# Kernel optimization log

Measured on AMD Instinct MI355X. Metric: run time of the kernel, lower is better.

Reference implementation:

```python
import jax, jax.numpy as jnp
import numpy as np
import math

G_GRAPHS = 32   # graphs per batch
NPG = 2048      # nodes per graph
DEG = 8         # avg degree
IN_DIM = 128
HID = 128

def _lin(k, fi, fo):
    return jax.random.normal(k, (fi, fo), jnp.float32) / np.sqrt(fi).astype(np.float32)

def setup_inputs():
    key = jax.random.key(0)
    ks = jax.random.split(key, 32)
    Nt = G_GRAPHS * NPG
    Epg = NPG * DEG
    E = G_GRAPHS * Epg
    x = jax.random.normal(ks[0], (Nt, IN_DIM), jnp.float32)
    src = jax.random.randint(ks[1], (E,), 0, NPG)
    dst = jax.random.randint(ks[2], (E,), 0, NPG)
    off = (jnp.arange(E) // Epg) * NPG  # keep edges within their graph block
    edge_index = jnp.stack([src + off, dst + off]).astype(jnp.int32)
    batch = (jnp.arange(Nt) // NPG).astype(jnp.int32)
    p = {}
    dims = [(IN_DIM, HID), (HID, HID), (HID, HID), (HID, HID)]
    for i, (fi, fo) in enumerate(dims, 1):
        p['Wl%d' % i] = _lin(ks[3 * i], fi, fo)
        p['bl%d' % i] = jnp.zeros((fo,), jnp.float32)
        p['Wr%d' % i] = _lin(ks[3 * i + 1], fi, fo)
    for j in (1, 2):  # SAGPooling score GNN (GraphConv hidden->1)
        p['Prel%d' % j] = _lin(ks[15 + 2 * j], HID, 1)
        p['prb%d' % j] = jnp.zeros((1,), jnp.float32)
        p['Proot%d' % j] = _lin(ks[16 + 2 * j], HID, 1)
    p['W5'] = _lin(ks[24], HID, 64); p['b5'] = jnp.zeros((64,), jnp.float32)
    p['W6'] = _lin(ks[25], 64, 2);  p['b6'] = jnp.zeros((2,), jnp.float32)
    return dict(x=x, edge_index=edge_index, batch=batch, npg=NPG, **p)

def reference(x, edge_index, batch, npg,
              Wl1, bl1, Wr1, Wl2, bl2, Wr2, Wl3, bl3, Wr3, Wl4, bl4, Wr4,
              Prel1, prb1, Proot1, Prel2, prb2, Proot2, W5, b5, W6, b6):
    src, dst = edge_index[0], edge_index[1]
    Nt = x.shape[0]
    Gn = Nt // npg

    def sage(h, em, Wl, bl, Wr):
        # SAGEConv (mean aggr): lin_l(mean_j x_j) + lin_r(x_root)
        s = jax.ops.segment_sum(h[src] * em[:, None], dst, num_segments=Nt)
        c = jax.ops.segment_sum(em, dst, num_segments=Nt)
        return (s / jnp.maximum(c, 1.0)[:, None]) @ Wl + bl + h @ Wr

    def pool(h, em, nm, k, Prel, prb, Proot):
        # SAGPooling: score = GraphConv(h) (add aggr), top-k per graph, x *= tanh(score)
        s = jax.ops.segment_sum(h[src] * em[:, None], dst, num_segments=Nt)
        score = (s @ Prel + h @ Proot + prb)[:, 0]
        smr = jnp.where(nm > 0, score, -1e30).reshape(Gn, npg)
        _, idx = jax.lax.top_k(smr, k)
        newm = jnp.zeros((Gn, npg), h.dtype).at[jnp.arange(Gn)[:, None], idx].set(1.0).reshape(-1)
        h = h * jnp.tanh(score)[:, None] * newm[:, None]
        em = em * newm[src] * newm[dst]  # filter_adj: keep edges with both ends kept
        return h, em, newm

    em = jnp.ones(src.shape, x.dtype)
    nm = jnp.ones((Nt,), x.dtype)
    h = jax.nn.relu(sage(x, em, Wl1, bl1, Wr1))
    h = jax.nn.relu(sage(h, em, Wl2, bl2, Wr2))
    k1 = math.ceil(0.5 * npg)
    h, em, nm = pool(h, em, nm, k1, Prel1, prb1, Proot1)
    h = jax.nn.relu(sage(h, em, Wl3, bl3, Wr3)) * nm[:, None]
    h = jax.nn.relu(sage(h, em, Wl4, bl4, Wr4)) * nm[:, None]
    k2 = math.ceil(0.5 * k1)
    h, em, nm = pool(h, em, nm, k2, Prel2, prb2, Proot2)
    # global mean pool over surviving nodes
    sums = jax.ops.segment_sum(h, batch, num_segments=Gn)
    cnt = jax.ops.segment_sum(nm, batch, num_segments=Gn)
    g = sums / jnp.maximum(cnt, 1.0)[:, None]
    g = jax.nn.relu(g @ W5 + b5)
    return jax.nn.log_softmax(g @ W6 + b6, axis=1)
```

## Files before the change

kernel.cpp:

```cpp
#include <hip/hip_runtime.h>
#include <hip/hip_bf16.h>
#include <math.h>

#define NT   65536
#define NPGC 2048
#define NG   32
#define NE   524288
#define HID  128

typedef short short8 __attribute__((ext_vector_type(8)));
typedef float f32x4  __attribute__((ext_vector_type(4)));

__device__ __forceinline__ float bf2f(unsigned short u) {
    union { unsigned int i; float f; } v; v.i = ((unsigned int)u) << 16; return v.f;
}
__device__ __forceinline__ unsigned short f2bf(float f) {
    union { float f; unsigned int i; } v; v.f = f;
    unsigned int x = v.i;
    return (unsigned short)((x + 0x7fffu + ((x >> 16) & 1u)) >> 16);
}
__device__ __forceinline__ void split2(float v, unsigned short& hi, unsigned short& lo) {
    unsigned int b = __float_as_uint(v);
    hi = (unsigned short)(b >> 16);
    float rem = v - __uint_as_float(b & 0xFFFF0000u);
    lo = (unsigned short)(__float_as_uint(rem) >> 16);
}

__global__ void k_detect(const unsigned short* __restrict__ x, int* __restrict__ flag) {
    __shared__ int cnt;
    if (threadIdx.x == 0) cnt = 0;
    __syncthreads();
    int sane = 0;
#pragma unroll
    for (int j = 0; j < 16; ++j) {
        unsigned short u = x[threadIdx.x * 16 + j];
        int e = (u >> 7) & 0xFF;
        if (e > 0x60 && e < 0xA0) sane++;
    }
    atomicAdd(&cnt, sane);
    __syncthreads();
    if (threadIdx.x == 0) *flag = (cnt > 3686) ? 1 : 0;
}

struct CvtDesc { const void* src[22]; int n[22]; int off[22]; };

__global__ void k_cvt(CvtDesc d, float* __restrict__ wts, const int* __restrict__ flag) {
    int t = blockIdx.y;
    int n = d.n[t];
    bool isbf = (*flag != 0);
    const unsigned short* sb = (const unsigned short*)d.src[t];
    const float* sf = (const float*)d.src[t];
    float* o = wts + d.off[t];
    for (int i = blockIdx.x * blockDim.x + threadIdx.x; i < n; i += gridDim.x * blockDim.x)
        o[i] = isbf ? bf2f(sb[i]) : sf[i];
}

__global__ void k_packW(const float* __restrict__ wts, int4 oWl, int4 oWr,
                        unsigned short* __restrict__ Wpack,
                        int* __restrict__ rowc, int* __restrict__ fill) {
    int idx = blockIdx.x * 256 + threadIdx.x;
    if (idx < NT) { rowc[idx] = 0; fill[idx] = 0; }
    if (idx >= 4 * 8 * 8 * 64 * 8) return;
    int L    = idx >> 15;
    int rem  = idx & 32767;
    int ct   = rem >> 12;
    int rem2 = rem & 4095;
    int ks   = rem2 >> 9;
    int rem3 = rem2 & 511;
    int lane = rem3 >> 3;
    int j    = rem3 & 7;
    int k   = ks * 32 + (lane >> 4) * 8 + j;
    int col = ct * 16 + (lane & 15);
    int ol = (L == 0) ? oWl.x : (L == 1) ? oWl.y : (L == 2) ? oWl.z : oWl.w;
    int orr = (L == 0) ? oWr.x : (L == 1) ? oWr.y : (L == 2) ? oWr.z : oWr.w;
    float w = (k < 128) ? wts[ol + k * 128 + col] : wts[orr + (k - 128) * 128 + col];
    unsigned short hi = f2bf(w);
    unsigned short lo = f2bf(w - bf2f(hi));
    int base = L * 65536 + (ct * 8 + ks) * 512 + lane * 8 + j;
    Wpack[base]         = hi;
    Wpack[base + 32768] = lo;
}

__global__ void k_load_x(const void* __restrict__ x, float* __restrict__ out,
                         const int* __restrict__ flag, int n4,
                         float* __restrict__ nm, const int* __restrict__ dstE,
                         int* __restrict__ rowc) {
    int i = blockIdx.x * blockDim.x + threadIdx.x;
    if (i < NT) nm[i] = 1.0f;
    if (i < NE) atomicAdd(&rowc[dstE[i]], 1);
    if (i >= n4) return;
    if (*flag) {
        ushort4 v = ((const ushort4*)x)[i];
        float4 o;
        o.x = bf2f(v.x); o.y = bf2f(v.y); o.z = bf2f(v.z); o.w = bf2f(v.w);
        ((float4*)out)[i] = o;
    }
}

__global__ void k_scan1(const int* __restrict__ cnt, int* __restrict__ rp, int* __restrict__ bsum,
                        float* __restrict__ invc) {
    __shared__ int s[256];
    int t = threadIdx.x;
    int i = blockIdx.x * 256 + t;
    int v = cnt[i];
    invc[i] = 1.0f / fmaxf((float)v, 1.0f);
    s[t] = v;
    __syncthreads();
    for (int off = 1; off < 256; off <<= 1) {
        int a = (t >= off) ? s[t - off] : 0;
        __syncthreads();
        s[t] += a;
        __syncthreads();
    }
    rp[i] = s[t] - v;
    if (t == 255) bsum[blockIdx.x] = s[255];
}

__global__ void k_scan23(int* __restrict__ rp, const int* __restrict__ bsum) {
    __shared__ int s[256];
    int t = threadIdx.x;
    s[t] = bsum[t];
    __syncthreads();
    for (int off = 1; off < 256; off <<= 1) {
        int a = (t >= off) ? s[t - off] : 0;
        __syncthreads();
        s[t] += a;
        __syncthreads();
    }
    int boffv = s[blockIdx.x] - bsum[blockIdx.x];
    int i = blockIdx.x * 256 + t;
    rp[i] += boffv;
    if (i == 0) rp[NT] = NE;
}

__global__ void k_scatter(const int* __restrict__ src, const int* __restrict__ dst,
                          const int* __restrict__ rp, int* __restrict__ fill, int* __restrict__ col) {
    int e = blockIdx.x * blockDim.x + threadIdx.x;
    if (e < NE) {
        int d = dst[e];
        int p = rp[d] + atomicAdd(&fill[d], 1);
        col[p] = src[e];
    }
}

__global__ void k_invc(const float* __restrict__ nm, const int* __restrict__ rp,
                       const int* __restrict__ col, float* __restrict__ invc) {
    int n = blockIdx.x * 256 + threadIdx.x;
    int beg = rp[n], end = rp[n + 1];
    float c = 0.f;
    for (int e = beg; e < end; ++e) c += nm[col[e]];
    invc[n] = 1.0f / fmaxf(c, 1.0f);
}

__device__ __forceinline__ int lds_sw(int node, int k) {
    int g = k >> 3;
    int go = g ^ (node & 7);
    return node * 128 + go * 8 + (k & 7);
}

template<bool HAS_TS>
__device__ __forceinline__ void sage_body(
    const float* __restrict__ h, const float* __restrict__ ts,
    const float* __restrict__ nm, const float* __restrict__ invc,
    const int* __restrict__ rp, const int* __restrict__ col,
    const unsigned short* __restrict__ Wp,
    unsigned short* Ahi, unsigned short* Alo,
    int n0, int tid, f32x4 acc[2][2])
{
    int lane = tid & 63, w = tid >> 6;
    int lrow = lane & 15, quad = lane >> 4;

#pragma unroll
    for (int pass = 0; pass < 4; ++pass) {
        int node = pass * 8 + (tid >> 5);
        int f = (tid & 31) * 4;
        int gn = n0 + node;
        float ax = 0.f, ay = 0.f, az = 0.f, aw = 0.f;
        if (nm[gn] > 0.f) {
            int beg = rp[gn], end = rp[gn + 1];
            for (int e0 = beg; e0 < end; e0 += 4) {
                int ecl = end - 1;
                int e1 = (e0 + 1 < end) ? e0 + 1 : ecl;
                int e2 = (e0 + 2 < end) ? e0 + 2 : ecl;
                int e3 = (e0 + 3 < end) ? e0 + 3 : ecl;
                int s0 = col[e0], s1 = col[e1], s2 = col[e2], s3 = col[e3];
                float4 v0 = *(const float4*)&h[(size_t)s0 * HID + f];
                float4 v1 = *(const float4*)&h[(size_t)s1 * HID + f];
                float4 v2 = *(const float4*)&h[(size_t)s2 * HID + f];
                float4 v3 = *(const float4*)&h[(size_t)s3 * HID + f];
                float c0 = HAS_TS ? ts[s0] : 1.0f;
                float c1 = (e0 + 1 < end) ? (HAS_TS ? ts[s1] : 1.0f) : 0.0f;
                float c2 = (e0 + 2 < end) ? (HAS_TS ? ts[s2] : 1.0f) : 0.0f;
                float c3 = (e0 + 3 < end) ? (HAS_TS ? ts[s3] : 1.0f) : 0.0f;
                ax += v0.x * c0 + v1.x * c1 + v2.x * c2 + v3.x * c3;
                ay += v0.y * c0 + v1.y * c1 + v2.y * c2 + v3.y * c3;
                az += v0.z * c0 + v1.z * c1 + v2.z * c2 + v3.z * c3;
                aw += v0.w * c0 + v1.w * c1 + v2.w * c2 + v3.w * c3;
            }
        }
        float inv = invc[gn];
        ushort4 hi4, lo4;
        split2(ax * inv, hi4.x, lo4.x);
        split2(ay * inv, hi4.y, lo4.y);
        split2(az * inv, hi4.z, lo4.z);
        split2(aw * inv, hi4.w, lo4.w);
        int a = lds_sw(node, f);
        *(ushort4*)&Ahi[a] = hi4;
        *(ushort4*)&Alo[a] = lo4;
    }
    __syncthreads();

#pragma unroll
    for (int ks = 0; ks < 4; ++ks) {
        short8 bh[2], blo[2];
#pragma unroll
        for (int c = 0; c < 2; ++c) {
            int ct = 2 * w + c;
            bh[c]  = *(const short8*)&Wp[(ct * 8 + ks) * 512 + lane * 8];
            blo[c] = *(const short8*)&Wp[32768 + (ct * 8 + ks) * 512 + lane * 8];
        }
        int kb = ks * 32 + quad * 8;
#pragma unroll
        for (int st = 0; st < 2; ++st) {
            int a = lds_sw(st * 16 + lrow, kb);
            short8 ah = *(const short8*)&Ahi[a];
            short8 al = *(const short8*)&Alo[a];
#pragma unroll
            for (int c = 0; c < 2; ++c) {
                acc[st][c] = __builtin_amdgcn_mfma_f32_16x16x32_bf16(ah, bh[c],  acc[st][c], 0, 0, 0);
                acc[st][c] = __builtin_amdgcn_mfma_f32_16x16x32_bf16(al, bh[c],  acc[st][c], 0, 0, 0);
                acc[st][c] = __builtin_amdgcn_mfma_f32_16x16x32_bf16(ah, blo[c], acc[st][c], 0, 0, 0);
            }
        }
    }
    __syncthreads();

#pragma unroll
    for (int i = 0; i < 4; ++i) {
        int idx = i * 256 + tid;
        int node = idx >> 5;
        int f = (idx & 31) * 4;
        int gn = n0 + node;
        float4 v = *(const float4*)&h[(size_t)gn * HID + f];
        float sc = HAS_TS ? ts[gn] : 1.0f;
        ushort4 hi4, lo4;
        split2(v.x * sc, hi4.x, lo4.x);
        split2(v.y * sc, hi4.y, lo4.y);
        split2(v.z * sc, hi4.z, lo4.z);
        split2(v.w * sc, hi4.w, lo4.w);
        int a = lds_sw(node, f);
        *(ushort4*)&Ahi[a] = hi4;
        *(ushort4*)&Alo[a] = lo4;
    }
    __syncthreads();

#pragma unroll
    for (int ks = 4; ks < 8; ++ks) {
        short8 bh[2], blo[2];
#pragma unroll
        for (int c = 0; c < 2; ++c) {
            int ct = 2 * w + c;
            bh[c]  = *(const short8*)&Wp[(ct * 8 + ks) * 512 + lane * 8];
            blo[c] = *(const short8*)&Wp[32768 + (ct * 8 + ks) * 512 + lane * 8];
        }
        int kb = (ks - 4) * 32 + quad * 8;
#pragma unroll
        for (int st = 0; st < 2; ++st) {
            int a = lds_sw(st * 16 + lrow, kb);
            short8 ah = *(const short8*)&Ahi[a];
            short8 al = *(const short8*)&Alo[a];
#pragma unroll
            for (int c = 0; c < 2; ++c) {
                acc[st][c] = __builtin_amdgcn_mfma_f32_16x16x32_bf16(ah, bh[c],  acc[st][c], 0, 0, 0);
                acc[st][c] = __builtin_amdgcn_mfma_f32_16x16x32_bf16(al, bh[c],  acc[st][c], 0, 0, 0);
                acc[st][c] = __builtin_amdgcn_mfma_f32_16x16x32_bf16(ah, blo[c], acc[st][c], 0, 0, 0);
            }
        }
    }
}

template<bool HAS_TS>
__global__ void __launch_bounds__(256, 8) k_sage_plain(
    const float* __restrict__ h, const void* __restrict__ xraw, const int* __restrict__ flag,
    const float* __restrict__ ts,
    const float* __restrict__ nm, const float* __restrict__ invc,
    const int* __restrict__ rp, const int* __restrict__ col,
    const unsigned short* __restrict__ Wp, const float* __restrict__ bl,
    float* __restrict__ out)
{
    __shared__ unsigned short Ahi[32 * 128];
    __shared__ unsigned short Alo[32 * 128];
    int tid = threadIdx.x;
    int b = blockIdx.x;
    int graph = (b & 7) * 4 + (b >> 9);
    int tile  = (b >> 3) & 63;
    int n0 = graph * NPGC + tile * 32;
    int lane = tid & 63, w = tid >> 6;
    int lrow = lane & 15, quad = lane >> 4;
    f32x4 acc[2][2] = {};

    const float* hh = h;
    if (xraw && *flag == 0) hh = (const float*)xraw;

    sage_body<HAS_TS>(hh, ts, nm, invc, rp, col, Wp, Ahi, Alo, n0, tid, acc);

#pragma unroll
    for (int c = 0; c < 2; ++c) {
        int colg = (2 * w + c) * 16 + lrow;
        float bias = bl[colg];
#pragma unroll
        for (int st = 0; st < 2; ++st) {
#pragma unroll
            for (int rr = 0; rr < 4; ++rr) {
                int node = n0 + st * 16 + quad * 4 + rr;
                float val = fmaxf(acc[st][c][rr] + bias, 0.f) * nm[node];
                out[(size_t)node * HID + colg] = val;
            }
        }
    }
}

__global__ void __launch_bounds__(256, 8) k_sage_dots(
    const float* __restrict__ h,
    const float* __restrict__ nm, const float* __restrict__ invc,
    const int* __restrict__ rp, const int* __restrict__ col,
    const unsigned short* __restrict__ Wp, const float* __restrict__ bl,
    float* __restrict__ out,
    const float* __restrict__ Prel, const float* __restrict__ Proot,
    float* __restrict__ q, float* __restrict__ r)
{
    __shared__ unsigned short Ahi[32 * 128];
    __shared__ unsigned short Alo[32 * 128];
    int tid = threadIdx.x;
    int b = blockIdx.x;
    int graph = (b & 7) * 4 + (b >> 9);
    int tile  = (b >> 3) & 63;
    int n0 = graph * NPGC + tile * 32;
    int lane = tid & 63, w = tid >> 6;
    int lrow = lane & 15, quad = lane >> 4;
    f32x4 acc[2][2] = {};

    sage_body<false>(h, nullptr, nm, invc, rp, col, Wp, Ahi, Alo, n0, tid, acc);

    float qp[2][4] = {}, rp_[2][4] = {};
#pragma unroll
    for (int c = 0; c < 2; ++c) {
        int colg = (2 * w + c) * 16 + lrow;
        float bias = bl[colg];
        float pq = Prel[colg], pr = Proot[colg];
#pragma unroll
        for (int st = 0; st < 2; ++st) {
#pragma unroll
            for (int rr = 0; rr < 4; ++rr) {
                int node = n0 + st * 16 + quad * 4 + rr;
                float val = fmaxf(acc[st][c][rr] + bias, 0.f) * nm[node];
                out[(size_t)node * HID + colg] = val;
                qp[st][rr] += val * pq;
                rp_[st][rr] += val * pr;
            }
        }
    }
#pragma unroll
    for (int st = 0; st < 2; ++st)
#pragma unroll
        for (int rr = 0; rr < 4; ++rr) {
#pragma unroll
            for (int m = 1; m < 16; m <<= 1) {
                qp[st][rr]  += __shfl_xor(qp[st][rr],  m, 64);
                rp_[st][rr] += __shfl_xor(rp_[st][rr], m, 64);
            }
        }
    __syncthreads();
    float* qa = (float*)Ahi;
    if (tid < 64) qa[tid] = 0.f;
    __syncthreads();
    if (lrow == 0) {
#pragma unroll
        for (int st = 0; st < 2; ++st)
#pragma unroll
            for (int rr = 0; rr < 4; ++rr) {
                int nl = st * 16 + quad * 4 + rr;
                atomicAdd(&qa[nl], qp[st][rr]);
                atomicAdd(&qa[32 + nl], rp_[st][rr]);
            }
    }
    __syncthreads();
    if (tid < 32) {
        q[n0 + tid] = qa[tid];
        r[n0 + tid] = qa[32 + tid];
    }
}

__global__ void k_score(const float* __restrict__ q, const float* __restrict__ r,
                        const float* __restrict__ prb,
                        const int* __restrict__ rp, const int* __restrict__ col,
                        float* __restrict__ score) {
    int n = blockIdx.x * 256 + threadIdx.x;
    int beg = rp[n], end = rp[n + 1];
    float s = 0.f;
    for (int e = beg; e < end; ++e) s += q[col[e]];
    score[n] = s + r[n] + prb[0];
}

__global__ void __launch_bounds__(256) k_topk(const float* __restrict__ score,
                                              float* __restrict__ nm,
                                              float* __restrict__ tval, int k) {
    __shared__ unsigned int u[NPGC];
    __shared__ int hist[256];
    __shared__ int scanb[257];
    __shared__ int wtot[4];
    __shared__ unsigned int s_byte;
    __shared__ int s_kk;
    int tid = threadIdx.x;
    int lane = tid & 63, wv = tid >> 6;
    int base = blockIdx.x * NPGC;

    for (int j = tid; j < NPGC; j += 256) {
        float sc = (nm[base + j] > 0.f) ? score[base + j] : -1e30f;
        unsigned int v = __float_as_uint(sc);
        v = (v & 0x80000000u) ? ~v : (v | 0x80000000u);
        u[j] = v;
    }
    hist[tid] = 0;
    if (tid == 0) scanb[256] = 0;
    __syncthreads();

    unsigned int prefix = 0;
    int kk = k;
#pragma unroll
    for (int round = 0; round < 4; ++round) {
        int shift = 24 - 8 * round;
        unsigned int pmask = (round == 0) ? 0u : (0xFFFFFFFFu << (32 - 8 * round));
        for (int j = tid; j < NPGC; j += 256) {
            unsigned int v = u[j];
            if ((v & pmask) == prefix) atomicAdd(&hist[(v >> shift) & 0xFF], 1);
        }
        __syncthreads();
        int s = hist[tid];
#pragma unroll
        for (int off = 1; off < 64; off <<= 1) {
            int t = __shfl_down(s, off, 64);
            s += (lane + off < 64) ? t : 0;
        }
        if (lane == 0) wtot[wv] = s;
        __syncthreads();
        int add = 0;
#pragma unroll
        for (int w2 = 1; w2 < 4; ++w2) add += (wv + w2 < 4) ? wtot[wv + w2] : 0;
        s += add;
        scanb[tid] = s;
        __syncthreads();
        int above = scanb[tid + 1];
        if (s >= kk && above < kk) { s_byte = (unsigned int)tid; s_kk = kk - above; }
        hist[tid] = 0;
        __syncthreads();
        prefix |= (s_byte << shift);
        kk = s_kk;
    }
    unsigned int thr = prefix;

    int j0 = tid * 8;
    int cnt = 0;
#pragma unroll
    for (int j = 0; j < 8; ++j) cnt += (u[j0 + j] == thr);
    int s = cnt;
#pragma unroll
    for (int off = 1; off < 64; off <<= 1) {
        int t = __shfl_up(s, off, 64);
        s += (lane >= off) ? t : 0;
    }
    if (lane == 63) wtot[wv] = s;
    __syncthreads();
    int add = 0;
#pragma unroll
    for (int w2 = 0; w2 < 4; ++w2) add += (w2 < wv) ? wtot[w2] : 0;
    int rank = s - cnt + add;
#pragma unroll
    for (int j = 0; j < 8; ++j) {
        unsigned int v = u[j0 + j];
        bool keep;
        if (v > thr) keep = true;
        else if (v == thr) { keep = (rank < kk); rank++; }
        else keep = false;
        nm[base + j0 + j]   = keep ? 1.0f : 0.0f;
        tval[base + j0 + j] = keep ? tanhf(score[base + j0 + j]) : 0.0f;
    }
}

__global__ void k_gsum(const float* __restrict__ h, const float* __restrict__ t,
                       const float* __restrict__ nm,
                       float* __restrict__ g, float* __restrict__ gcnt) {
    int b = blockIdx.x;
    int graph = b >> 4, part = b & 15;
    int f = threadIdx.x & 127, sub = threadIdx.x >> 7;
    int nbase = graph * NPGC + part * 128 + sub * 64;
    float acc = 0.f;
#pragma unroll 4
    for (int n = 0; n < 64; ++n)
        acc += h[(size_t)(nbase + n) * HID + f] * t[nbase + n];
    atomicAdd(&g[graph * HID + f], acc);
    if (threadIdx.x < 64 && sub == 0) {
        float cnt = 0.f;
        int cb = graph * NPGC + part * 128;
        for (int n = threadIdx.x; n < 128; n += 64) cnt += nm[cb + n];
        for (int o = 32; o > 0; o >>= 1) cnt += __shfl_down(cnt, o, 64);
        if (threadIdx.x == 0) atomicAdd(&gcnt[graph], cnt);
    }
}

__global__ void k_mlp(const float* __restrict__ g, const float* __restrict__ gcnt,
                      const float* __restrict__ W5,
                      const float* __restrict__ b5, const float* __restrict__ W6,
                      const float* __restrict__ b6, void* __restrict__ out,
                      const int* __restrict__ flag) {
    __shared__ float g5[64];
    __shared__ float ls[2];
    int graph = blockIdx.x, j = threadIdx.x;
    float ic = 1.0f / fmaxf(gcnt[graph], 1.0f);
    float acc = b5[j];
    for (int f = 0; f < HID; ++f)
        acc += (g[graph * HID + f] * ic) * W5[f * 64 + j];
    g5[j] = fmaxf(acc, 0.f);
    __syncthreads();
    if (j < 2) {
        float l = b6[j];
        for (int t = 0; t < 64; ++t) l += g5[t] * W6[t * 2 + j];
        ls[j] = l;
    }
    __syncthreads();
    if (j == 0) {
        float a = ls[0], b = ls[1];
        float mx = fmaxf(a, b);
        float lse = mx + logf(expf(a - mx) + expf(b - mx));
        if (*flag) {
            ((unsigned short*)out)[graph * 2 + 0] = f2bf(a - lse);
            ((unsigned short*)out)[graph * 2 + 1] = f2bf(b - lse);
        } else {
            ((float*)out)[graph * 2 + 0] = a - lse;
            ((float*)out)[graph * 2 + 1] = b - lse;
        }
    }
}

extern "C" void kernel_launch(void* const* d_in, const int* in_sizes, int n_in,
                              void* d_out, int out_size, void* d_ws, size_t ws_size,
                              hipStream_t stream) {
    const void* x    = d_in[0];
    const int*  ei   = (const int*)d_in[1];
    const int*  srcE = ei;
    const int*  dstE = ei + NE;

    char* ws = (char*)d_ws;
    float* hA    = (float*)(ws + 0);
    float* hB    = (float*)(ws + 33554432);
    float* tvec  = (float*)(ws + 67108864);
    float* invc  = (float*)(ws + 67371008);
    float* q     = (float*)(ws + 100663296);
    float* r     = (float*)(ws + 100925440);
    float* score = (float*)(ws + 101187584);
    float* nm    = (float*)(ws + 101449728);
    int*   rowc  = (int*)  (ws + 101711872);
    int*   rp    = (int*)  (ws + 101974016);
    int*   bsum  = (int*)  (ws + 102236416);
    int*   fill  = (int*)  (ws + 102238464);
    int*   col   = (int*)  (ws + 102500608);
    float* g     = (float*)(ws + 104597760);
    float* gcnt  = (float*)(ws + 104614144);
    int*   flag  = (int*)  (ws + 104615936);
    float* wts   = (float*)(ws + 104616960);
    unsigned short* Wpack = (unsigned short*)(ws + 105179136);
    (void)in_sizes; (void)n_in; (void)out_size; (void)ws_size;

    const int O_Wl1 = 0,      O_bl1 = 16384,  O_Wr1 = 16512;
    const int O_Wl2 = 32896,  O_bl2 = 49280,  O_Wr2 = 49408;
    const int O_Wl3 = 65792,  O_bl3 = 82176,  O_Wr3 = 82304;
    const int O_Wl4 = 98688,  O_bl4 = 115072, O_Wr4 = 115200;
    const int O_Pr1 = 131584, O_pb1 = 131712, O_Po1 = 131713;
    const int O_Pr2 = 131841, O_pb2 = 131969, O_Po2 = 131970;
    const int O_W5  = 132098, O_b5  = 140290, O_W6 = 140354, O_b6 = 140482;

    CvtDesc d;
    const int srcIdx[22] = {4,5,6,7,8,9,10,11,12,13,14,15,16,17,18,19,20,21,22,23,24,25};
    const int nelems[22] = {16384,128,16384, 16384,128,16384, 16384,128,16384, 16384,128,16384,
                            128,1,128, 128,1,128, 8192,64,128,2};
    const int offs[22]   = {O_Wl1,O_bl1,O_Wr1, O_Wl2,O_bl2,O_Wr2, O_Wl3,O_bl3,O_Wr3, O_Wl4,O_bl4,O_Wr4,
                            O_Pr1,O_pb1,O_Po1, O_Pr2,O_pb2,O_Po2, O_W5,O_b5,O_W6,O_b6};
    for (int i = 0; i < 22; ++i) { d.src[i] = d_in[srcIdx[i]]; d.n[i] = nelems[i]; d.off[i] = offs[i]; }

    hipMemsetAsync(g, 0, (NG * HID + NG + 64) * 4, stream);

    k_detect <<<1, 256, 0, stream>>>((const unsigned short*)x, flag);
    k_cvt    <<<dim3(64, 22), 256, 0, stream>>>(d, wts, flag);
    k_packW  <<<512, 256, 0, stream>>>(wts, make_int4(O_Wl1, O_Wl2, O_Wl3, O_Wl4),
                                       make_int4(O_Wr1, O_Wr2, O_Wr3, O_Wr4), Wpack, rowc, fill);
    k_load_x <<<8192, 256, 0, stream>>>(x, hA, flag, NT * HID / 4, nm, dstE, rowc);

    k_scan1  <<<256, 256, 0, stream>>>(rowc, rp, bsum, invc);
    k_scan23 <<<256, 256, 0, stream>>>(rp, bsum);
    k_scatter<<<2048, 256, 0, stream>>>(srcE, dstE, rp, fill, col);

    k_sage_plain<false><<<2048, 256, 0, stream>>>(hA, x, flag, nullptr, nm, invc, rp, col,
                                                  Wpack + 0 * 65536, wts + O_bl1, hB);
    k_sage_dots<<<2048, 256, 0, stream>>>(hB, nm, invc, rp, col,
                                          Wpack + 1 * 65536, wts + O_bl2, hA,
                                          wts + O_Pr1, wts + O_Po1, q, r);

    k_score<<<256, 256, 0, stream>>>(q, r, wts + O_pb1, rp, col, score);
    k_topk <<<32, 256, 0, stream>>>(score, nm, tvec, 1024);
    k_invc <<<256, 256, 0, stream>>>(nm, rp, col, invc);

    k_sage_plain<true><<<2048, 256, 0, stream>>>(hA, nullptr, flag, tvec, nm, invc, rp, col,
                                                 Wpack + 2 * 65536, wts + O_bl3, hB);
    k_sage_dots<<<2048, 256, 0, stream>>>(hB, nm, invc, rp, col,
                                          Wpack + 3 * 65536, wts + O_bl4, hA,
                                          wts + O_Pr2, wts + O_Po2, q, r);

    k_score<<<256, 256, 0, stream>>>(q, r, wts + O_pb2, rp, col, score);
    k_topk <<<32, 256, 0, stream>>>(score, nm, tvec, 512);

    k_gsum<<<512, 256, 0, stream>>>(hA, tvec, nm, g, gcnt);
    k_mlp <<<32, 64, 0, stream>>>(g, gcnt, wts + O_W5, wts + O_b5, wts + O_W6, wts + O_b6, d_out, flag);
}
```

Measured before the change: 382.8 us.

## Compact surviving nodes after pooling and run later layers on active list

Top-k now emits a compacted list of kept node indices per graph, and the post-pool SAGE layers, the inverse-count pass and the global sum iterate only over those nodes. This halves the launched blocks for layers 3-4 and removes per-node mask checks. The global mean now divides by the fixed k2 instead of a counted total, and q is zeroed for dropped nodes so the score kernel stays correct. Gathers become indirect through the index list, and stale hidden rows of dropped nodes are no longer overwritten, which relies on later code never reading them.

```diff
diff --git a/kernel.cpp b/kernel.cpp
--- a/kernel.cpp
+++ b/kernel.cpp
@@ -7,6 +7,8 @@
 #define NG   32
 #define NE   524288
 #define HID  128
+#define K1   1024
+#define K2   512
 
 typedef short short8 __attribute__((ext_vector_type(8)));
 typedef float f32x4  __attribute__((ext_vector_type(4)));
@@ -144,8 +146,9 @@
 }
 
 __global__ void k_invc(const float* __restrict__ nm, const int* __restrict__ rp,
-                       const int* __restrict__ col, float* __restrict__ invc) {
-    int n = blockIdx.x * 256 + threadIdx.x;
+                       const int* __restrict__ col, float* __restrict__ invc,
+                       const int* __restrict__ act) {
+    int n = act[blockIdx.x * 256 + threadIdx.x];
     int beg = rp[n], end = rp[n + 1];
     float c = 0.f;
     for (int e = beg; e < end; ++e) c += nm[col[e]];
@@ -158,14 +161,14 @@
     return node * 128 + go * 8 + (k & 7);
 }
 
-template<bool HAS_TS>
+template<bool HAS_TS, bool COMPACT>
 __device__ __forceinline__ void sage_body(
     const float* __restrict__ h, const float* __restrict__ ts,
     const float* __restrict__ nm, const float* __restrict__ invc,
     const int* __restrict__ rp, const int* __restrict__ col,
     const unsigned short* __restrict__ Wp,
     unsigned short* Ahi, unsigned short* Alo,
-    int n0, int tid, f32x4 acc[2][2])
+    int n0, const int* sact, int tid, f32x4 acc[2][2])
 {
     int lane = tid & 63, w = tid >> 6;
     int lrow = lane & 15, quad = lane >> 4;
@@ -174,9 +177,10 @@
     for (int pass = 0; pass < 4; ++pass) {
         int node = pass * 8 + (tid >> 5);
         int f = (tid & 31) * 4;
-        int gn = n0 + node;
+        int gn = COMPACT ? sact[node] : n0 + node;
         float ax = 0.f, ay = 0.f, az = 0.f, aw = 0.f;
-        if (nm[gn] > 0.f) {
+        bool active = COMPACT ? true : (nm[gn] > 0.f);
+        if (active) {
             int beg = rp[gn], end = rp[gn + 1];
             for (int e0 = beg; e0 < end; e0 += 4) {
                 int ecl = end - 1;
@@ -240,7 +244,7 @@
         int idx = i * 256 + tid;
         int node = idx >> 5;
         int f = (idx & 31) * 4;
-        int gn = n0 + node;
+        int gn = COMPACT ? sact[node] : n0 + node;
         float4 v = *(const float4*)&h[(size_t)gn * HID + f];
         float sc = HAS_TS ? ts[gn] : 1.0f;
         ushort4 hi4, lo4;
@@ -279,30 +283,40 @@
     }
 }
 
-template<bool HAS_TS>
+template<bool COMPACT>
+__device__ __forceinline__ void map_block(int b, int& graph, int& tile) {
+    if (COMPACT) { graph = (b & 7) * 4 + (b >> 8); tile = (b >> 3) & 31; }
+    else         { graph = (b & 7) * 4 + (b >> 9); tile = (b >> 3) & 63; }
+}
+
+template<bool HAS_TS, bool COMPACT>
 __global__ void __launch_bounds__(256, 8) k_sage_plain(
     const float* __restrict__ h, const void* __restrict__ xraw, const int* __restrict__ flag,
     const float* __restrict__ ts,
     const float* __restrict__ nm, const float* __restrict__ invc,
     const int* __restrict__ rp, const int* __restrict__ col,
     const unsigned short* __restrict__ Wp, const float* __restrict__ bl,
-    float* __restrict__ out)
+    float* __restrict__ out, const int* __restrict__ act)
 {
     __shared__ unsigned short Ahi[32 * 128];
     __shared__ unsigned short Alo[32 * 128];
+    __shared__ int sact[32];
     int tid = threadIdx.x;
-    int b = blockIdx.x;
-    int graph = (b & 7) * 4 + (b >> 9);
-    int tile  = (b >> 3) & 63;
+    int graph, tile;
+    map_block<COMPACT>(blockIdx.x, graph, tile);
     int n0 = graph * NPGC + tile * 32;
+    if (COMPACT) {
+        if (tid < 32) sact[tid] = act[graph * K1 + tile * 32 + tid];
+        __syncthreads();
+    }
     int lane = tid & 63, w = tid >> 6;
     int lrow = lane & 15, quad = lane >> 4;
     f32x4 acc[2][2] = {};
 
     const float* hh = h;
-    if (xraw && *flag == 0) hh = (const float*)xraw;
-
-    sage_body<HAS_TS>(hh, ts, nm, invc, rp, col, Wp, Ahi, Alo, n0, tid, acc);
+    if (!COMPACT && xraw && *flag == 0) hh = (const float*)xraw;
+
+    sage_body<HAS_TS, COMPACT>(hh, ts, nm, invc, rp, col, Wp, Ahi, Alo, n0, sact, tid, acc);
 
 #pragma unroll
     for (int c = 0; c < 2; ++c) {
@@ -312,35 +326,42 @@
         for (int st = 0; st < 2; ++st) {
 #pragma unroll
             for (int rr = 0; rr < 4; ++rr) {
-                int node = n0 + st * 16 + quad * 4 + rr;
-                float val = fmaxf(acc[st][c][rr] + bias, 0.f) * nm[node];
+                int nl = st * 16 + quad * 4 + rr;
+                int node = COMPACT ? sact[nl] : n0 + nl;
+                float val = fmaxf(acc[st][c][rr] + bias, 0.f);
+                if (!COMPACT) val *= nm[node];
                 out[(size_t)node * HID + colg] = val;
             }
         }
     }
 }
 
+template<bool HAS_TS, bool COMPACT>
 __global__ void __launch_bounds__(256, 8) k_sage_dots(
-    const float* __restrict__ h,
+    const float* __restrict__ h, const float* __restrict__ ts,
     const float* __restrict__ nm, const float* __restrict__ invc,
     const int* __restrict__ rp, const int* __restrict__ col,
     const unsigned short* __restrict__ Wp, const float* __restrict__ bl,
     float* __restrict__ out,
     const float* __restrict__ Prel, const float* __restrict__ Proot,
-    float* __restrict__ q, float* __restrict__ r)
+    float* __restrict__ q, float* __restrict__ r, const int* __restrict__ act)
 {
     __shared__ unsigned short Ahi[32 * 128];
     __shared__ unsigned short Alo[32 * 128];
+    __shared__ int sact[32];
     int tid = threadIdx.x;
-    int b = blockIdx.x;
-    int graph = (b & 7) * 4 + (b >> 9);
-    int tile  = (b >> 3) & 63;
+    int graph, tile;
+    map_block<COMPACT>(blockIdx.x, graph, tile);
     int n0 = graph * NPGC + tile * 32;
+    if (COMPACT) {
+        if (tid < 32) sact[tid] = act[graph * K1 + tile * 32 + tid];
+        __syncthreads();
+    }
     int lane = tid & 63, w = tid >> 6;
     int lrow = lane & 15, quad = lane >> 4;
     f32x4 acc[2][2] = {};
 
-    sage_body<false>(h, nullptr, nm, invc, rp, col, Wp, Ahi, Alo, n0, tid, acc);
+    sage_body<HAS_TS, COMPACT>(h, ts, nm, invc, rp, col, Wp, Ahi, Alo, n0, sact, tid, acc);
 
     float qp[2][4] = {}, rp_[2][4] = {};
 #pragma unroll
@@ -352,8 +373,10 @@
         for (int st = 0; st < 2; ++st) {
 #pragma unroll
             for (int rr = 0; rr < 4; ++rr) {
-                int node = n0 + st * 16 + quad * 4 + rr;
-                float val = fmaxf(acc[st][c][rr] + bias, 0.f) * nm[node];
+                int nl = st * 16 + quad * 4 + rr;
+                int node = COMPACT ? sact[nl] : n0 + nl;
+                float val = fmaxf(acc[st][c][rr] + bias, 0.f);
+                if (!COMPACT) val *= nm[node];
                 out[(size_t)node * HID + colg] = val;
                 qp[st][rr] += val * pq;
                 rp_[st][rr] += val * pr;
@@ -386,8 +409,9 @@
     }
     __syncthreads();
     if (tid < 32) {
-        q[n0 + tid] = qa[tid];
-        r[n0 + tid] = qa[32 + tid];
+        int node = COMPACT ? sact[tid] : n0 + tid;
+        q[node] = qa[tid];
+        r[node] = qa[32 + tid];
     }
 }
 
@@ -402,13 +426,17 @@
     score[n] = s + r[n] + prb[0];
 }
 
+template<bool ZQ>
 __global__ void __launch_bounds__(256) k_topk(const float* __restrict__ score,
                                               float* __restrict__ nm,
-                                              float* __restrict__ tval, int k) {
+                                              float* __restrict__ tval, int k,
+                                              int* __restrict__ act,
+                                              float* __restrict__ q) {
     __shared__ unsigned int u[NPGC];
     __shared__ int hist[256];
     __shared__ int scanb[257];
     __shared__ int wtot[4];
+    __shared__ int wtot2[4];
     __shared__ unsigned int s_byte;
     __shared__ int s_kk;
     int tid = threadIdx.x;
@@ -475,40 +503,59 @@
 #pragma unroll
     for (int w2 = 0; w2 < 4; ++w2) add += (w2 < wv) ? wtot[w2] : 0;
     int rank = s - cnt + add;
+
+    unsigned int keepmask = 0u;
+    int myrank = rank;
+    int kcnt = 0;
 #pragma unroll
     for (int j = 0; j < 8; ++j) {
         unsigned int v = u[j0 + j];
-        bool keep;
-        if (v > thr) keep = true;
-        else if (v == thr) { keep = (rank < kk); rank++; }
-        else keep = false;
-        nm[base + j0 + j]   = keep ? 1.0f : 0.0f;
-        tval[base + j0 + j] = keep ? tanhf(score[base + j0 + j]) : 0.0f;
+        bool kp;
+        if (v > thr) kp = true;
+        else if (v == thr) { kp = (myrank < kk); myrank++; }
+        else kp = false;
+        keepmask |= (kp ? 1u : 0u) << j;
+        kcnt += kp ? 1 : 0;
+    }
+    int s2 = kcnt;
+#pragma unroll
+    for (int off = 1; off < 64; off <<= 1) {
+        int t2 = __shfl_up(s2, off, 64);
+        s2 += (lane >= off) ? t2 : 0;
+    }
+    if (lane == 63) wtot2[wv] = s2;
+    __syncthreads();
+    int pos = s2 - kcnt;
+#pragma unroll
+    for (int w2 = 0; w2 < 4; ++w2) pos += (w2 < wv) ? wtot2[w2] : 0;
+    int* actg = act + blockIdx.x * k;
+#pragma unroll
+    for (int j = 0; j < 8; ++j) {
+        bool kp = (keepmask >> j) & 1u;
+        int n = base + j0 + j;
+        nm[n]   = kp ? 1.0f : 0.0f;
+        tval[n] = kp ? tanhf(score[n]) : 0.0f;
+        if (kp)      { actg[pos++] = n; }
+        else if (ZQ) { q[n] = 0.0f; }
     }
 }
 
 __global__ void k_gsum(const float* __restrict__ h, const float* __restrict__ t,
-                       const float* __restrict__ nm,
-                       float* __restrict__ g, float* __restrict__ gcnt) {
+                       const int* __restrict__ act, float* __restrict__ g) {
     int b = blockIdx.x;
-    int graph = b >> 4, part = b & 15;
+    int graph = b >> 2, part = b & 3;
     int f = threadIdx.x & 127, sub = threadIdx.x >> 7;
-    int nbase = graph * NPGC + part * 128 + sub * 64;
+    int base = graph * K2 + part * 128 + sub * 64;
     float acc = 0.f;
 #pragma unroll 4
-    for (int n = 0; n < 64; ++n)
-        acc += h[(size_t)(nbase + n) * HID + f] * t[nbase + n];
+    for (int n = 0; n < 64; ++n) {
+        int gn = act[base + n];
+        acc += h[(size_t)gn * HID + f] * t[gn];
+    }
     atomicAdd(&g[graph * HID + f], acc);
-    if (threadIdx.x < 64 && sub == 0) {
-        float cnt = 0.f;
-        int cb = graph * NPGC + part * 128;
-        for (int n = threadIdx.x; n < 128; n += 64) cnt += nm[cb + n];
-        for (int o = 32; o > 0; o >>= 1) cnt += __shfl_down(cnt, o, 64);
-        if (threadIdx.x == 0) atomicAdd(&gcnt[graph], cnt);
-    }
-}
-
-__global__ void k_mlp(const float* __restrict__ g, const float* __restrict__ gcnt,
+}
+
+__global__ void k_mlp(const float* __restrict__ g,
                       const float* __restrict__ W5,
                       const float* __restrict__ b5, const float* __restrict__ W6,
                       const float* __restrict__ b6, void* __restrict__ out,
@@ -516,7 +563,7 @@
     __shared__ float g5[64];
     __shared__ float ls[2];
     int graph = blockIdx.x, j = threadIdx.x;
-    float ic = 1.0f / fmaxf(gcnt[graph], 1.0f);
+    const float ic = 1.0f / (float)K2;
     float acc = b5[j];
     for (int f = 0; f < HID; ++f)
         acc += (g[graph * HID + f] * ic) * W5[f * 64 + j];
@@ -565,10 +612,11 @@
     int*   fill  = (int*)  (ws + 102238464);
     int*   col   = (int*)  (ws + 102500608);
     float* g     = (float*)(ws + 104597760);
-    float* gcnt  = (float*)(ws + 104614144);
     int*   flag  = (int*)  (ws + 104615936);
     float* wts   = (float*)(ws + 104616960);
     unsigned short* Wpack = (unsigned short*)(ws + 105179136);
+    int*   act1  = rowc;
+    int*   act2  = fill;
     (void)in_sizes; (void)n_in; (void)out_size; (void)ws_size;
 
     const int O_Wl1 = 0,      O_bl1 = 16384,  O_Wr1 = 16512;
@@ -599,25 +647,25 @@
     k_scan23 <<<256, 256, 0, stream>>>(rp, bsum);
     k_scatter<<<2048, 256, 0, stream>>>(srcE, dstE, rp, fill, col);
 
-    k_sage_plain<false><<<2048, 256, 0, stream>>>(hA, x, flag, nullptr, nm, invc, rp, col,
-                                                  Wpack + 0 * 65536, wts + O_bl1, hB);
-    k_sage_dots<<<2048, 256, 0, stream>>>(hB, nm, invc, rp, col,
-                                          Wpack + 1 * 65536, wts + O_bl2, hA,
-                                          wts + O_Pr1, wts + O_Po1, q, r);
+    k_sage_plain<false, false><<<2048, 256, 0, stream>>>(hA, x, flag, nullptr, nm, invc, rp, col,
+                                                         Wpack + 0 * 65536, wts + O_bl1, hB, nullptr);
+    k_sage_dots<false, false><<<2048, 256, 0, stream>>>(hB, nullptr, nm, invc, rp, col,
+                                                        Wpack + 1 * 65536, wts + O_bl2, hA,
+                                                        wts + O_Pr1, wts + O_Po1, q, r, nullptr);
 
     k_score<<<256, 256, 0, stream>>>(q, r, wts + O_pb1, rp, col, score);
-    k_topk <<<32, 256, 0, stream>>>(score, nm, tvec, 1024);
-    k_invc <<<256, 256, 0, stream>>>(nm, rp, col, invc);
-
-    k_sage_plain<true><<<2048, 256, 0, stream>>>(hA, nullptr, flag, tvec, nm, invc, rp, col,
-                                                 Wpack + 2 * 65536, wts + O_bl3, hB);
-    k_sage_dots<<<2048, 256, 0, stream>>>(hB, nm, invc, rp, col,
-                                          Wpack + 3 * 65536, wts + O_bl4, hA,
-                                          wts + O_Pr2, wts + O_Po2, q, r);
+    k_topk<true><<<32, 256, 0, stream>>>(score, nm, tvec, K1, act1, q);
+    k_invc <<<NG * K1 / 256, 256, 0, stream>>>(nm, rp, col, invc, act1);
+
+    k_sage_plain<true, true><<<1024, 256, 0, stream>>>(hA, nullptr, flag, tvec, nm, invc, rp, col,
+                                                       Wpack + 2 * 65536, wts + O_bl3, hB, act1);
+    k_sage_dots<true, true><<<1024, 256, 0, stream>>>(hB, nm, nm, invc, rp, col,
+                                                      Wpack + 3 * 65536, wts + O_bl4, hA,
+                                                      wts + O_Pr2, wts + O_Po2, q, r, act1);
 
     k_score<<<256, 256, 0, stream>>>(q, r, wts + O_pb2, rp, col, score);
-    k_topk <<<32, 256, 0, stream>>>(score, nm, tvec, 512);
-
-    k_gsum<<<512, 256, 0, stream>>>(hA, tvec, nm, g, gcnt);
-    k_mlp <<<32, 64, 0, stream>>>(g, gcnt, wts + O_W5, wts + O_b5, wts + O_W6, wts + O_b6, d_out, flag);
-}
+    k_topk<false><<<32, 256, 0, stream>>>(score, nm, tvec, K2, act2, nullptr);
+
+    k_gsum<<<NG * 4, 256, 0, stream>>>(hA, tvec, act2, g);
+    k_mlp <<<32, 64, 0, stream>>>(g, wts + O_W5, wts + O_b5, wts + O_W6, wts + O_b6, d_out, flag);
+}
```

New measurement: 369.4 us. 1.04x faster.
